# Kernel tuning notes

Measured on AMD Instinct MI355X. Metric: run time of the kernel, lower is better.

The kernel has to match this reference:

```python
import jax, jax.numpy as jnp
import numpy as np

N_NODES = 100000
N_EDGES = 3200000
D_FEAT = 128


def setup_inputs() -> dict:
    key = jax.random.key(0)
    k1, k2, k3, k4 = jax.random.split(key, 4)
    edge_row = jax.random.randint(k1, (N_EDGES,), 0, N_NODES, dtype=jnp.int64 if jax.config.jax_enable_x64 else jnp.int32)
    edge_col = jax.random.randint(k2, (N_EDGES,), 0, N_NODES, dtype=edge_row.dtype)
    edge_val = jax.random.uniform(k3, (N_EDGES,), dtype=jnp.float32)
    embeds = jax.random.normal(k4, (N_NODES, D_FEAT), dtype=jnp.float32)
    return {"edge_row": edge_row, "edge_col": edge_col, "edge_val": edge_val, "embeds": embeds}


def reference(edge_row, edge_col, edge_val, embeds):
    # SpMM: out[r] = sum_{e: row(e)=r} val(e) * embeds[col(e)]
    messages = edge_val[:, None] * embeds[edge_col]  # [E, D]
    out = jax.ops.segment_sum(messages, edge_row, num_segments=embeds.shape[0])  # [N, D]
    return out
```

## Files before the change

kernel.cpp:

```cpp
#include <hip/hip_runtime.h>
#include <hip/hip_bf16.h>
#include <stdint.h>

#define N_NODES 100000
#define D_FEAT  128
#define RSH     6
#define RPB     64
#define NBUCK   ((N_NODES + RPB - 1) / RPB)
#define OCAP    8192
#define SC_THR  1024
#define SC_EPT  16
#define SC_TILE (SC_THR * SC_EPT)
#define COLMASK 0x1FFFF

__device__ __forceinline__ uint32_t bf16_rne(float x) {
    uint32_t u = __float_as_uint(x);
    return (u + 0x7FFFu + ((u >> 16) & 1u)) >> 16;
}

template <int CAPF_, bool PAD, bool CONV>
__global__ __launch_bounds__(SC_THR) void scatter_conv_kernel(
    const int* __restrict__ row, const int* __restrict__ col,
    const float* __restrict__ val, int* __restrict__ cursor,
    int2* __restrict__ rec, int4* __restrict__ oflow, int* __restrict__ ocnt,
    const float4* __restrict__ embf, uint2* __restrict__ embbf,
    int n, int scb, int n4)
{
    if (CONV && (int)blockIdx.x >= scb) {
        const int nb = gridDim.x - scb;
        const int stride = nb * SC_THR;
        for (int i = (blockIdx.x - scb) * SC_THR + threadIdx.x; i < n4; i += stride) {
            float4 f = embf[i];
            embbf[i] = make_uint2(bf16_rne(f.x) | (bf16_rne(f.y) << 16),
                                  bf16_rne(f.z) | (bf16_rne(f.w) << 16));
        }
        return;
    }

    __shared__ int cnt[NBUCK];
    __shared__ int base[NBUCK];
    const int tid = threadIdx.x;
    const int e0  = blockIdx.x * SC_TILE + tid * SC_EPT;

    for (int i = tid; i < NBUCK; i += SC_THR) cnt[i] = 0;
    __syncthreads();

    int   r[SC_EPT], c[SC_EPT];
    float v[SC_EPT];
    if (e0 + SC_EPT <= n) {
        const int4* rp = (const int4*)(row + e0);
        const int4* cp = (const int4*)(col + e0);
        const float4* vp = (const float4*)(val + e0);
        #pragma unroll
        for (int q = 0; q < SC_EPT / 4; q++) {
            int4 rr = rp[q]; int4 cc = cp[q]; float4 vv = vp[q];
            r[q*4+0]=rr.x; r[q*4+1]=rr.y; r[q*4+2]=rr.z; r[q*4+3]=rr.w;
            c[q*4+0]=cc.x; c[q*4+1]=cc.y; c[q*4+2]=cc.z; c[q*4+3]=cc.w;
            v[q*4+0]=vv.x; v[q*4+1]=vv.y; v[q*4+2]=vv.z; v[q*4+3]=vv.w;
        }
    } else {
        #pragma unroll
        for (int k = 0; k < SC_EPT; k++) {
            int e = e0 + k;
            if (e < n) { r[k] = row[e]; c[k] = col[e]; v[k] = val[e]; }
            else       { r[k] = -1; }
        }
    }

    int rk[SC_EPT];
    #pragma unroll
    for (int k = 0; k < SC_EPT; k++)
        if (r[k] >= 0) rk[k] = atomicAdd(&cnt[r[k] >> RSH], 1);
    __syncthreads();

    for (int i = tid; i < NBUCK; i += SC_THR) {
        int cc = cnt[i];
        if (cc) {
            int padded = PAD ? ((cc + 7) & ~7) : cc;
            int b0 = atomicAdd(&cursor[i], padded);
            base[i] = b0;
            if (PAD) {
                int2* slab = rec + (size_t)i * CAPF_;
                for (int p = cc; p < padded; ++p) {
                    int pos = b0 + p;
                    if (pos < CAPF_) slab[pos] = make_int2(0, 0);
                }
            }
        }
    }
    __syncthreads();

    #pragma unroll
    for (int k = 0; k < SC_EPT; k++) {
        if (r[k] >= 0) {
            int bk  = r[k] >> RSH;
            int pos = base[bk] + rk[k];
            if (pos < CAPF_) {
                rec[(size_t)bk * CAPF_ + pos] =
                    make_int2(((r[k] & (RPB - 1)) << 17) | c[k], __float_as_int(v[k]));
            } else {
                int op = atomicAdd(ocnt, 1);
                if (op < OCAP) oflow[op] = make_int4(r[k], c[k], __float_as_int(v[k]), 0);
            }
        }
    }
}

template <bool BF16, int CAPF_>
__global__ __launch_bounds__(512) void spmm_fixed_kernel(const int* __restrict__ fill,
                                                         const int2* __restrict__ rec,
                                                         const void* __restrict__ emb,
                                                         float* __restrict__ out)
{
    constexpr int KMAX = (CAPF_ + 511) / 512;
    __shared__ int2 buf[CAPF_];
    __shared__ int  cnt[RPB];
    __shared__ int  start[RPB];
    __shared__ int  sc_[RPB];

    const int tid  = threadIdx.x;
    const int lane = tid & 63;
    const int wv   = tid >> 6;
    const int b    = blockIdx.x;
    const int m    = min(fill[b], CAPF_);
    const int rows = min(RPB, N_NODES - b * RPB);
    const size_t beg = (size_t)b * CAPF_;
    const uint32_t* __restrict__ embu = (const uint32_t*)emb;
    const float2*   __restrict__ emb2 = (const float2*)emb;

    if (tid < RPB) cnt[tid] = 0;
    __syncthreads();

    int2 rc[KMAX];
    int  rk[KMAX];
    #pragma unroll
    for (int k = 0; k < KMAX; k++) {
        int i = k * 512 + tid;
        if (i < m) {
            rc[k] = rec[beg + i];
            rk[k] = atomicAdd(&cnt[rc[k].x >> 17], 1);
        }
    }
    __syncthreads();
    if (tid < RPB) sc_[tid] = cnt[tid];
    __syncthreads();
    for (int off = 1; off < RPB; off <<= 1) {
        int t = 0;
        if (tid < RPB && tid >= off) t = sc_[tid - off];
        __syncthreads();
        if (tid < RPB) sc_[tid] += t;
        __syncthreads();
    }
    if (tid < RPB) start[tid] = sc_[tid] - cnt[tid];
    __syncthreads();
    #pragma unroll
    for (int k = 0; k < KMAX; k++) {
        int i = k * 512 + tid;
        if (i < m) buf[start[rc[k].x >> 17] + rk[k]] = rc[k];
    }
    __syncthreads();

    for (int rl = wv * 8; rl < wv * 8 + 8; rl++) {
        const int s0 = start[rl];
        const int c0 = cnt[rl];
        float ax = 0.f, ay = 0.f;
        int j = 0;
        for (; j + 8 <= c0; j += 8) {
            int2 e[8];
            #pragma unroll
            for (int q = 0; q < 8; q++) e[q] = buf[s0 + j + q];
            float mx[8], my[8], vv[8];
            #pragma unroll
            for (int q = 0; q < 8; q++) {
                int cc = e[q].x & COLMASK;
                vv[q] = __int_as_float(e[q].y);
                if (BF16) {
                    uint32_t u = embu[(size_t)cc * 64 + lane];
                    mx[q] = __uint_as_float(u << 16);
                    my[q] = __uint_as_float(u & 0xFFFF0000u);
                } else {
                    float2 mm = emb2[(size_t)cc * 64 + lane];
                    mx[q] = mm.x; my[q] = mm.y;
                }
            }
            #pragma unroll
            for (int q = 0; q < 8; q++) { ax += vv[q] * mx[q]; ay += vv[q] * my[q]; }
        }
        for (; j < c0; j++) {
            int2 e = buf[s0 + j];
            int cc = e.x & COLMASK;
            float vv = __int_as_float(e.y);
            float mx, my;
            if (BF16) {
                uint32_t u = embu[(size_t)cc * 64 + lane];
                mx = __uint_as_float(u << 16);
                my = __uint_as_float(u & 0xFFFF0000u);
            } else {
                float2 mm = emb2[(size_t)cc * 64 + lane];
                mx = mm.x; my = mm.y;
            }
            ax += vv * mx; ay += vv * my;
        }
        if (rl < rows) {
            float2* o = (float2*)(out + (size_t)(b * RPB + rl) * D_FEAT);
            o[lane] = make_float2(ax, ay);
        }
    }
}

__global__ __launch_bounds__(256) void oflow_kernel(const int4* __restrict__ oflow,
                                                    const int* __restrict__ ocnt,
                                                    const float* __restrict__ embeds,
                                                    float* __restrict__ out) {
    const int nof  = min(*ocnt, OCAP);
    const int lane = threadIdx.x & 63;
    const int w    = (blockIdx.x * 256 + threadIdx.x) >> 6;
    const int nw   = (gridDim.x * 256) >> 6;
    for (int i = w; i < nof; i += nw) {
        int4 e = oflow[i];
        const float2* src = (const float2*)(embeds + (size_t)e.y * D_FEAT);
        float2 mm = src[lane];
        float vv = __int_as_float(e.z);
        float* dst = out + (size_t)e.x * D_FEAT + (lane << 1);
        unsafeAtomicAdd(dst,     vv * mm.x);
        unsafeAtomicAdd(dst + 1, vv * mm.y);
    }
}

__global__ __launch_bounds__(256) void spmm_atomic_kernel(
    const int* __restrict__ edge_row, const int* __restrict__ edge_col,
    const float* __restrict__ edge_val, const float* __restrict__ embeds,
    float* __restrict__ out, int n_edges)
{
    const int lane    = threadIdx.x & 63;
    const int wave_id = (blockIdx.x * blockDim.x + threadIdx.x) >> 6;
    const int n_waves = (gridDim.x * blockDim.x) >> 6;
    for (int e = wave_id; e < n_edges; e += n_waves) {
        const int   rr = edge_row[e];
        const int   cc = edge_col[e];
        const float vv = edge_val[e];
        const float2* src = (const float2*)(embeds + (size_t)cc * D_FEAT);
        float2 mm = src[lane];
        float* dst = out + (size_t)rr * D_FEAT + (lane << 1);
        unsafeAtomicAdd(dst,     vv * mm.x);
        unsafeAtomicAdd(dst + 1, vv * mm.y);
    }
}

static inline size_t align256(size_t x) { return (x + 255) & ~(size_t)255; }

extern "C" void kernel_launch(void* const* d_in, const int* in_sizes, int n_in,
                              void* d_out, int out_size, void* d_ws, size_t ws_size,
                              hipStream_t stream) {
    const int*   edge_row = (const int*)d_in[0];
    const int*   edge_col = (const int*)d_in[1];
    const float* edge_val = (const float*)d_in[2];
    const float* embeds   = (const float*)d_in[3];
    float*       out      = (float*)d_out;

    const int n_edges = in_sizes[0];
    const int scb = (n_edges + SC_TILE - 1) / SC_TILE;
    const int n4  = N_NODES * (D_FEAT / 4);

    const size_t sz_cur   = align256((size_t)(NBUCK + 1) * 4);
    const size_t sz_oflow = align256((size_t)OCAP * 16);
    const size_t sz_rec_p = align256((size_t)NBUCK * 3072 * 8);
    const size_t sz_rec_c = align256((size_t)NBUCK * 2304 * 8);
    const size_t sz_emb   = align256((size_t)N_NODES * 64 * 4);

    const size_t need_pad  = sz_cur + sz_oflow + sz_rec_p + sz_emb;
    const size_t need_comp = sz_cur + sz_oflow + sz_rec_c + sz_emb;
    const size_t need_fp32 = sz_cur + sz_oflow + sz_rec_c;

    if (ws_size < need_fp32) {
        hipMemsetAsync(out, 0, (size_t)out_size * sizeof(float), stream);
        spmm_atomic_kernel<<<dim3(4096), dim3(256), 0, stream>>>(
            edge_row, edge_col, edge_val, embeds, out, n_edges);
        return;
    }

    char* ws = (char*)d_ws;
    int*  cursor = (int*)ws;
    int*  ocnt   = cursor + NBUCK;
    int4* oflow  = (int4*)(ws + sz_cur);

    hipMemsetAsync(cursor, 0, (size_t)(NBUCK + 1) * 4, stream);

    if (ws_size >= need_pad) {
        int2*     rec   = (int2*)(ws + sz_cur + sz_oflow);
        uint32_t* embbf = (uint32_t*)(ws + sz_cur + sz_oflow + sz_rec_p);
        scatter_conv_kernel<3072, true, true><<<dim3(scb * 2), dim3(SC_THR), 0, stream>>>(
            edge_row, edge_col, edge_val, cursor, rec, oflow, ocnt,
            (const float4*)embeds, (uint2*)embbf, n_edges, scb, n4);
        spmm_fixed_kernel<true, 3072><<<dim3(NBUCK), dim3(512), 0, stream>>>(
            cursor, rec, embbf, out);
    } else if (ws_size >= need_comp) {
        int2*     rec   = (int2*)(ws + sz_cur + sz_oflow);
        uint32_t* embbf = (uint32_t*)(ws + sz_cur + sz_oflow + sz_rec_c);
        scatter_conv_kernel<2304, false, true><<<dim3(scb * 2), dim3(SC_THR), 0, stream>>>(
            edge_row, edge_col, edge_val, cursor, rec, oflow, ocnt,
            (const float4*)embeds, (uint2*)embbf, n_edges, scb, n4);
        spmm_fixed_kernel<true, 2304><<<dim3(NBUCK), dim3(512), 0, stream>>>(
            cursor, rec, embbf, out);
    } else {
        int2* rec = (int2*)(ws + sz_cur + sz_oflow);
        scatter_conv_kernel<2304, false, false><<<dim3(scb), dim3(SC_THR), 0, stream>>>(
            edge_row, edge_col, edge_val, cursor, rec, oflow, ocnt,
            (const float4*)embeds, (uint2*)nullptr, n_edges, scb, n4);
        spmm_fixed_kernel<false, 2304><<<dim3(NBUCK), dim3(512), 0, stream>>>(
            cursor, rec, embeds, out);
    }
    oflow_kernel<<<dim3(16), dim3(256), 0, stream>>>(oflow, ocnt, embeds, out);
}
```

Measured before the change: 328.8 us.

## Replace one-pass bucket scatter with two-pass radix partition and smaller row buckets

Result: faster. 304.9 us (-7.3%).

```diff
diff --git a/kernel.cpp b/kernel.cpp
--- a/kernel.cpp
+++ b/kernel.cpp
@@ -4,13 +4,22 @@
 
 #define N_NODES 100000
 #define D_FEAT  128
-#define RSH     6
-#define RPB     64
-#define NBUCK   ((N_NODES + RPB - 1) / RPB)
+#define RPB     32
+#define RSH     5
+#define SBSH    10
+#define SBROWS  1024
+#define NSUP    98
+#define NBUCKR  3125
+#define NBUCKF  3136
+#define SEGA    208
+#define REGF    320
+#define NREG    4
+#define CAPFF   (NREG*REGF)
+#define CAPFM   1152
 #define OCAP    8192
 #define SC_THR  1024
 #define SC_EPT  16
-#define SC_TILE (SC_THR * SC_EPT)
+#define SC_TILE (SC_THR*SC_EPT)
 #define COLMASK 0x1FFFF
 
 __device__ __forceinline__ uint32_t bf16_rne(float x) {
@@ -18,8 +27,111 @@
     return (u + 0x7FFFu + ((u >> 16) & 1u)) >> 16;
 }
 
-template <int CAPF_, bool PAD, bool CONV>
-__global__ __launch_bounds__(SC_THR) void scatter_conv_kernel(
+template <bool CONV>
+__global__ __launch_bounds__(SC_THR) void passA_kernel(
+    const int* __restrict__ row, const int* __restrict__ col,
+    const float* __restrict__ val, int* __restrict__ cntA,
+    int2* __restrict__ recA, int4* __restrict__ oflow, int* __restrict__ ocnt,
+    const float4* __restrict__ embf, uint2* __restrict__ embbf,
+    int n, int scb, int capa, int n4)
+{
+    if (CONV && (int)blockIdx.x >= scb) {
+        const int nb = gridDim.x - scb;
+        for (int i = (blockIdx.x - scb) * SC_THR + threadIdx.x; i < n4; i += nb * SC_THR) {
+            float4 f = embf[i];
+            embbf[i] = make_uint2(bf16_rne(f.x) | (bf16_rne(f.y) << 16),
+                                  bf16_rne(f.z) | (bf16_rne(f.w) << 16));
+        }
+        return;
+    }
+
+    __shared__ int cnt[NSUP];
+    const int tid = threadIdx.x;
+    const int w   = blockIdx.x;
+    for (int i = tid; i < NSUP; i += SC_THR) cnt[i] = 0;
+    __syncthreads();
+
+    const int e0 = w * SC_TILE + tid * SC_EPT;
+    #pragma unroll
+    for (int qq = 0; qq < SC_EPT / 4; qq++) {
+        const int e = e0 + qq * 4;
+        int r[4]; int c[4]; float v[4];
+        if (e + 4 <= n) {
+            int4 rr = *(const int4*)(row + e);
+            int4 cc = *(const int4*)(col + e);
+            float4 vv = *(const float4*)(val + e);
+            r[0]=rr.x; r[1]=rr.y; r[2]=rr.z; r[3]=rr.w;
+            c[0]=cc.x; c[1]=cc.y; c[2]=cc.z; c[3]=cc.w;
+            v[0]=vv.x; v[1]=vv.y; v[2]=vv.z; v[3]=vv.w;
+        } else {
+            #pragma unroll
+            for (int j = 0; j < 4; j++) {
+                if (e + j < n) { r[j] = row[e+j]; c[j] = col[e+j]; v[j] = val[e+j]; }
+                else r[j] = -1;
+            }
+        }
+        #pragma unroll
+        for (int j = 0; j < 4; j++) {
+            if (r[j] >= 0) {
+                const int sb = r[j] >> SBSH;
+                const int rk = atomicAdd(&cnt[sb], 1);
+                if (rk < SEGA) {
+                    recA[(size_t)sb * capa + w * SEGA + rk] =
+                        make_int2(((r[j] & (SBROWS - 1)) << 17) | c[j], __float_as_int(v[j]));
+                } else {
+                    int op = atomicAdd(ocnt, 1);
+                    if (op < OCAP) oflow[op] = make_int4(r[j], c[j], __float_as_int(v[j]), 0);
+                }
+            }
+        }
+    }
+    __syncthreads();
+    for (int i = tid; i < NSUP; i += SC_THR) cntA[i * scb + w] = min(cnt[i], SEGA);
+}
+
+__global__ __launch_bounds__(1024) void passB_kernel(
+    const int* __restrict__ cntA, const int2* __restrict__ recA,
+    int* __restrict__ fillF, int2* __restrict__ recF,
+    int4* __restrict__ oflow, int* __restrict__ ocnt,
+    int scb, int capa, int spq)
+{
+    __shared__ int cntB[32];
+    __shared__ int segc[64];
+    const int tid = threadIdx.x;
+    const int sb  = blockIdx.x >> 2;
+    const int q   = blockIdx.x & 3;
+    const int s0  = q * spq;
+    const int sq  = min(spq, scb - s0);
+    if (tid < 32) cntB[tid] = 0;
+    if (tid < sq) segc[tid] = cntA[sb * scb + s0 + tid];
+    __syncthreads();
+
+    const int sg = tid >> 8;
+    const int p  = tid & 255;
+    for (int it = 0; it * 4 < sq; it++) {
+        const int s = it * 4 + sg;
+        if (s < sq && p < segc[s]) {
+            int2 rcd = recA[(size_t)sb * capa + (size_t)(s0 + s) * SEGA + p];
+            const int rl10 = rcd.x >> 17;
+            const int bkl  = rl10 >> RSH;
+            const int rk   = atomicAdd(&cntB[bkl], 1);
+            const int bkg  = sb * 32 + bkl;
+            if (rk < REGF) {
+                recF[(size_t)bkg * CAPFF + q * REGF + rk] =
+                    make_int2(((rl10 & (RPB - 1)) << 17) | (rcd.x & COLMASK), rcd.y);
+            } else {
+                int op = atomicAdd(ocnt, 1);
+                if (op < OCAP)
+                    oflow[op] = make_int4(sb * SBROWS + rl10, rcd.x & COLMASK, rcd.y, 0);
+            }
+        }
+    }
+    __syncthreads();
+    if (tid < 32) fillF[(sb * 32 + tid) * NREG + q] = min(cntB[tid], REGF);
+}
+
+template <bool CONV>
+__global__ __launch_bounds__(SC_THR) void scatter_mid_kernel(
     const int* __restrict__ row, const int* __restrict__ col,
     const float* __restrict__ val, int* __restrict__ cursor,
     int2* __restrict__ rec, int4* __restrict__ oflow, int* __restrict__ ocnt,
@@ -28,25 +140,21 @@
 {
     if (CONV && (int)blockIdx.x >= scb) {
         const int nb = gridDim.x - scb;
-        const int stride = nb * SC_THR;
-        for (int i = (blockIdx.x - scb) * SC_THR + threadIdx.x; i < n4; i += stride) {
+        for (int i = (blockIdx.x - scb) * SC_THR + threadIdx.x; i < n4; i += nb * SC_THR) {
             float4 f = embf[i];
             embbf[i] = make_uint2(bf16_rne(f.x) | (bf16_rne(f.y) << 16),
                                   bf16_rne(f.z) | (bf16_rne(f.w) << 16));
         }
         return;
     }
-
-    __shared__ int cnt[NBUCK];
-    __shared__ int base[NBUCK];
+    __shared__ int cnt[NBUCKR];
+    __shared__ int base[NBUCKR];
     const int tid = threadIdx.x;
     const int e0  = blockIdx.x * SC_TILE + tid * SC_EPT;
-
-    for (int i = tid; i < NBUCK; i += SC_THR) cnt[i] = 0;
-    __syncthreads();
-
-    int   r[SC_EPT], c[SC_EPT];
-    float v[SC_EPT];
+    for (int i = tid; i < NBUCKR; i += SC_THR) cnt[i] = 0;
+    __syncthreads();
+
+    int r[SC_EPT], c[SC_EPT]; float v[SC_EPT];
     if (e0 + SC_EPT <= n) {
         const int4* rp = (const int4*)(row + e0);
         const int4* cp = (const int4*)(col + e0);
@@ -63,40 +171,26 @@
         for (int k = 0; k < SC_EPT; k++) {
             int e = e0 + k;
             if (e < n) { r[k] = row[e]; c[k] = col[e]; v[k] = val[e]; }
-            else       { r[k] = -1; }
-        }
-    }
-
+            else r[k] = -1;
+        }
+    }
     int rk[SC_EPT];
     #pragma unroll
     for (int k = 0; k < SC_EPT; k++)
         if (r[k] >= 0) rk[k] = atomicAdd(&cnt[r[k] >> RSH], 1);
     __syncthreads();
-
-    for (int i = tid; i < NBUCK; i += SC_THR) {
+    for (int i = tid; i < NBUCKR; i += SC_THR) {
         int cc = cnt[i];
-        if (cc) {
-            int padded = PAD ? ((cc + 7) & ~7) : cc;
-            int b0 = atomicAdd(&cursor[i], padded);
-            base[i] = b0;
-            if (PAD) {
-                int2* slab = rec + (size_t)i * CAPF_;
-                for (int p = cc; p < padded; ++p) {
-                    int pos = b0 + p;
-                    if (pos < CAPF_) slab[pos] = make_int2(0, 0);
-                }
-            }
-        }
-    }
-    __syncthreads();
-
+        if (cc) base[i] = atomicAdd(&cursor[i], cc);
+    }
+    __syncthreads();
     #pragma unroll
     for (int k = 0; k < SC_EPT; k++) {
         if (r[k] >= 0) {
-            int bk  = r[k] >> RSH;
+            int bk = r[k] >> RSH;
             int pos = base[bk] + rk[k];
-            if (pos < CAPF_) {
-                rec[(size_t)bk * CAPF_ + pos] =
+            if (pos < CAPFM) {
+                rec[(size_t)bk * CAPFM + pos] =
                     make_int2(((r[k] & (RPB - 1)) << 17) | c[k], __float_as_int(v[k]));
             } else {
                 int op = atomicAdd(ocnt, 1);
@@ -106,14 +200,16 @@
     }
 }
 
-template <bool BF16, int CAPF_>
-__global__ __launch_bounds__(512) void spmm_fixed_kernel(const int* __restrict__ fill,
-                                                         const int2* __restrict__ rec,
-                                                         const void* __restrict__ emb,
-                                                         float* __restrict__ out)
+template <bool BF16, int NREG_, int REGF_>
+__global__ __launch_bounds__(256) void spmm_kernel(const int* __restrict__ fills,
+                                                   const int2* __restrict__ rec,
+                                                   const void* __restrict__ emb,
+                                                   float* __restrict__ out)
 {
-    constexpr int KMAX = (CAPF_ + 511) / 512;
-    __shared__ int2 buf[CAPF_];
+    constexpr int CAP_ = NREG_ * REGF_;
+    constexpr int KR   = (REGF_ + 255) / 256;
+    constexpr int NS   = NREG_ * KR;
+    __shared__ int2 buf[CAP_];
     __shared__ int  cnt[RPB];
     __shared__ int  start[RPB];
     __shared__ int  sc_[RPB];
@@ -122,23 +218,27 @@
     const int lane = tid & 63;
     const int wv   = tid >> 6;
     const int b    = blockIdx.x;
-    const int m    = min(fill[b], CAPF_);
     const int rows = min(RPB, N_NODES - b * RPB);
-    const size_t beg = (size_t)b * CAPF_;
     const uint32_t* __restrict__ embu = (const uint32_t*)emb;
     const float2*   __restrict__ emb2 = (const float2*)emb;
 
     if (tid < RPB) cnt[tid] = 0;
     __syncthreads();
 
-    int2 rc[KMAX];
-    int  rk[KMAX];
+    int2 rc[NS];
+    int  rk[NS];
     #pragma unroll
-    for (int k = 0; k < KMAX; k++) {
-        int i = k * 512 + tid;
-        if (i < m) {
-            rc[k] = rec[beg + i];
-            rk[k] = atomicAdd(&cnt[rc[k].x >> 17], 1);
+    for (int q = 0; q < NREG_; q++) {
+        const int mq = min(fills[b * NREG_ + q], REGF_);
+        #pragma unroll
+        for (int k = 0; k < KR; k++) {
+            const int slot = q * KR + k;
+            const int i = k * 256 + tid;
+            rk[slot] = -1;
+            if (i < mq) {
+                rc[slot] = rec[(size_t)b * CAP_ + q * REGF_ + i];
+                rk[slot] = atomicAdd(&cnt[rc[slot].x >> 17], 1);
+            }
         }
     }
     __syncthreads();
@@ -154,10 +254,8 @@
     if (tid < RPB) start[tid] = sc_[tid] - cnt[tid];
     __syncthreads();
     #pragma unroll
-    for (int k = 0; k < KMAX; k++) {
-        int i = k * 512 + tid;
-        if (i < m) buf[start[rc[k].x >> 17] + rk[k]] = rc[k];
-    }
+    for (int slot = 0; slot < NS; slot++)
+        if (rk[slot] >= 0) buf[start[rc[slot].x >> 17] + rk[slot]] = rc[slot];
     __syncthreads();
 
     for (int rl = wv * 8; rl < wv * 8 + 8; rl++) {
@@ -259,56 +357,81 @@
     float*       out      = (float*)d_out;
 
     const int n_edges = in_sizes[0];
-    const int scb = (n_edges + SC_TILE - 1) / SC_TILE;
-    const int n4  = N_NODES * (D_FEAT / 4);
-
-    const size_t sz_cur   = align256((size_t)(NBUCK + 1) * 4);
-    const size_t sz_oflow = align256((size_t)OCAP * 16);
-    const size_t sz_rec_p = align256((size_t)NBUCK * 3072 * 8);
-    const size_t sz_rec_c = align256((size_t)NBUCK * 2304 * 8);
-    const size_t sz_emb   = align256((size_t)N_NODES * 64 * 4);
-
-    const size_t need_pad  = sz_cur + sz_oflow + sz_rec_p + sz_emb;
-    const size_t need_comp = sz_cur + sz_oflow + sz_rec_c + sz_emb;
-    const size_t need_fp32 = sz_cur + sz_oflow + sz_rec_c;
-
-    if (ws_size < need_fp32) {
+    const int scb  = (n_edges + SC_TILE - 1) / SC_TILE;
+    const int capa = scb * SEGA;
+    const int spq  = (scb + NREG - 1) / NREG;
+    const int n4   = N_NODES * (D_FEAT / 4);
+
+    size_t off = 0;
+    size_t o_meta  = off; off = align256(off + 256);
+    size_t o_oflow = off; off = align256(off + (size_t)OCAP * 16);
+    size_t o_fillF = off; off = align256(off + (size_t)NBUCKF * NREG * 4);
+    size_t o_cntA  = off; off = align256(off + (size_t)NSUP * scb * 4);
+    size_t o_recA  = off; off = align256(off + (size_t)NSUP * capa * 8);
+    size_t o_recF  = off; off = align256(off + (size_t)NBUCKF * CAPFF * 8);
+    size_t o_embF  = off; off = align256(off + (size_t)N_NODES * 64 * 4);
+    const size_t need_fast = off;
+    size_t mo = 0;
+    size_t m_meta  = mo; mo = align256(mo + 256);
+    size_t m_oflow = mo; mo = align256(mo + (size_t)OCAP * 16);
+    size_t m_cur   = mo; mo = align256(mo + (size_t)NBUCKR * 4);
+    size_t m_rec   = mo; mo = align256(mo + (size_t)NBUCKR * CAPFM * 8);
+    const size_t need_fp32 = mo;
+    size_t m_emb   = mo; mo = align256(mo + (size_t)N_NODES * 64 * 4);
+    const size_t need_mid = mo;
+
+    char* ws = (char*)d_ws;
+
+    if (ws_size >= need_fast) {
+        int*      ocnt  = (int*)(ws + o_meta);
+        int4*     oflow = (int4*)(ws + o_oflow);
+        int*      fillF = (int*)(ws + o_fillF);
+        int*      cntA  = (int*)(ws + o_cntA);
+        int2*     recA  = (int2*)(ws + o_recA);
+        int2*     recF  = (int2*)(ws + o_recF);
+        uint32_t* embbf = (uint32_t*)(ws + o_embF);
+
+        hipMemsetAsync(ocnt, 0, 256, stream);
+        passA_kernel<true><<<dim3(scb * 2), dim3(SC_THR), 0, stream>>>(
+            edge_row, edge_col, edge_val, cntA, recA, oflow, ocnt,
+            (const float4*)embeds, (uint2*)embbf, n_edges, scb, capa, n4);
+        passB_kernel<<<dim3(NSUP * NREG), dim3(1024), 0, stream>>>(
+            cntA, recA, fillF, recF, oflow, ocnt, scb, capa, spq);
+        spmm_kernel<true, NREG, REGF><<<dim3(NBUCKF), dim3(256), 0, stream>>>(
+            fillF, recF, embbf, out);
+        oflow_kernel<<<dim3(16), dim3(256), 0, stream>>>(oflow, ocnt, embeds, out);
+    } else if (ws_size >= need_mid) {
+        int*      ocnt  = (int*)(ws + m_meta);
+        int4*     oflow = (int4*)(ws + m_oflow);
+        int*      cur   = (int*)(ws + m_cur);
+        int2*     rec   = (int2*)(ws + m_rec);
+        uint32_t* embbf = (uint32_t*)(ws + m_emb);
+
+        hipMemsetAsync(ocnt, 0, 256, stream);
+        hipMemsetAsync(cur, 0, (size_t)NBUCKR * 4, stream);
+        scatter_mid_kernel<true><<<dim3(scb * 2), dim3(SC_THR), 0, stream>>>(
+            edge_row, edge_col, edge_val, cur, rec, oflow, ocnt,
+            (const float4*)embeds, (uint2*)embbf, n_edges, scb, n4);
+        spmm_kernel<true, 1, CAPFM><<<dim3(NBUCKR), dim3(256), 0, stream>>>(
+            cur, rec, embbf, out);
+        oflow_kernel<<<dim3(16), dim3(256), 0, stream>>>(oflow, ocnt, embeds, out);
+    } else if (ws_size >= need_fp32) {
+        int*  ocnt  = (int*)(ws + m_meta);
+        int4* oflow = (int4*)(ws + m_oflow);
+        int*  cur   = (int*)(ws + m_cur);
+        int2* rec   = (int2*)(ws + m_rec);
+
+        hipMemsetAsync(ocnt, 0, 256, stream);
+        hipMemsetAsync(cur, 0, (size_t)NBUCKR * 4, stream);
+        scatter_mid_kernel<false><<<dim3(scb), dim3(SC_THR), 0, stream>>>(
+            edge_row, edge_col, edge_val, cur, rec, oflow, ocnt,
+            (const float4*)embeds, (uint2*)nullptr, n_edges, scb, n4);
+        spmm_kernel<false, 1, CAPFM><<<dim3(NBUCKR), dim3(256), 0, stream>>>(
+            cur, rec, embeds, out);
+        oflow_kernel<<<dim3(16), dim3(256), 0, stream>>>(oflow, ocnt, embeds, out);
+    } else {
         hipMemsetAsync(out, 0, (size_t)out_size * sizeof(float), stream);
         spmm_atomic_kernel<<<dim3(4096), dim3(256), 0, stream>>>(
             edge_row, edge_col, edge_val, embeds, out, n_edges);
-        return;
-    }
-
-    char* ws = (char*)d_ws;
-    int*  cursor = (int*)ws;
-    int*  ocnt   = cursor + NBUCK;
-    int4* oflow  = (int4*)(ws + sz_cur);
-
-    hipMemsetAsync(cursor, 0, (size_t)(NBUCK + 1) * 4, stream);
-
-    if (ws_size >= need_pad) {
-        int2*     rec   = (int2*)(ws + sz_cur + sz_oflow);
-        uint32_t* embbf = (uint32_t*)(ws + sz_cur + sz_oflow + sz_rec_p);
-        scatter_conv_kernel<3072, true, true><<<dim3(scb * 2), dim3(SC_THR), 0, stream>>>(
-            edge_row, edge_col, edge_val, cursor, rec, oflow, ocnt,
-            (const float4*)embeds, (uint2*)embbf, n_edges, scb, n4);
-        spmm_fixed_kernel<true, 3072><<<dim3(NBUCK), dim3(512), 0, stream>>>(
-            cursor, rec, embbf, out);
-    } else if (ws_size >= need_comp) {
-        int2*     rec   = (int2*)(ws + sz_cur + sz_oflow);
-        uint32_t* embbf = (uint32_t*)(ws + sz_cur + sz_oflow + sz_rec_c);
-        scatter_conv_kernel<2304, false, true><<<dim3(scb * 2), dim3(SC_THR), 0, stream>>>(
-            edge_row, edge_col, edge_val, cursor, rec, oflow, ocnt,
-            (const float4*)embeds, (uint2*)embbf, n_edges, scb, n4);
-        spmm_fixed_kernel<true, 2304><<<dim3(NBUCK), dim3(512), 0, stream>>>(
-            cursor, rec, embbf, out);
-    } else {
-        int2* rec = (int2*)(ws + sz_cur + sz_oflow);
-        scatter_conv_kernel<2304, false, false><<<dim3(scb), dim3(SC_THR), 0, stream>>>(
-            edge_row, edge_col, edge_val, cursor, rec, oflow, ocnt,
-            (const float4*)embeds, (uint2*)nullptr, n_edges, scb, n4);
-        spmm_fixed_kernel<false, 2304><<<dim3(NBUCK), dim3(512), 0, stream>>>(
-            cursor, rec, embeds, out);
-    }
-    oflow_kernel<<<dim3(16), dim3(256), 0, stream>>>(oflow, ocnt, embeds, out);
-}
+    }
+}
```
